# Kernel optimization log

Measured on AMD Instinct MI355X. Metric: run time of the kernel, lower is better.

Reference implementation:

```python
import jax, jax.numpy as jnp
import numpy as np

N = 20000      # nodes
E = 320000     # edges (avg in-degree 16)
R = 100        # relation types
F = 256        # in_ent_feats == out_ent_feats == in_rel_feats
H = 8          # heads
D = F // H     # head dim = 32
HOP = 5        # PPR hops
ALPHA = 0.1
SLOPE = 0.2    # LeakyReLU negative slope


def _ln(x, g, b, eps=1e-5):
    m = x.mean(-1, keepdims=True)
    v = ((x - m) ** 2).mean(-1, keepdims=True)
    return (x - m) / jnp.sqrt(v + eps) * g + b


def setup_inputs() -> dict:
    key = jax.random.key(0)
    ks = jax.random.split(key, 12)
    s = 1.0 / np.sqrt(F)
    ent_feat = jax.random.normal(ks[0], (N, F), jnp.float32)
    rel_feat = jax.random.normal(ks[1], (R, F), jnp.float32)
    W_head = jax.random.normal(ks[2], (F, F), jnp.float32) * s
    W_tail = jax.random.normal(ks[3], (F, F), jnp.float32) * s
    W_ent = jax.random.normal(ks[4], (F, F), jnp.float32) * s
    W_rel = jax.random.normal(ks[5], (F, F), jnp.float32) * s
    attn = jax.random.normal(ks[6], (1, H, D), jnp.float32) * s
    ln_ent_g = jnp.ones((F,), jnp.float32); ln_ent_b = jnp.zeros((F,), jnp.float32)
    ln_rel_g = jnp.ones((F,), jnp.float32); ln_rel_b = jnp.zeros((F,), jnp.float32)
    ln_ff_g = jnp.ones((F,), jnp.float32); ln_ff_b = jnp.zeros((F,), jnp.float32)
    W1 = jax.random.normal(ks[7], (F, 4 * F), jnp.float32) * s
    b1 = jnp.zeros((4 * F,), jnp.float32)
    W2 = jax.random.normal(ks[8], (4 * F, F), jnp.float32) * (0.5 * s)
    b2 = jnp.zeros((F,), jnp.float32)
    src = jax.random.randint(ks[9], (E,), 0, N, dtype=jnp.int32)
    # every node must have in-degree >= 1 (DGL raises on 0-in-degree nodes)
    dst = jnp.concatenate([jnp.arange(N, dtype=jnp.int32),
                           jax.random.randint(ks[10], (E - N,), 0, N, dtype=jnp.int32)])
    rid = jax.random.randint(ks[11], (E,), 0, R, dtype=jnp.int32)
    return {"ent_feat": ent_feat, "rel_feat": rel_feat,
            "W_head": W_head, "W_tail": W_tail, "W_ent": W_ent, "W_rel": W_rel,
            "attn": attn,
            "ln_ent_g": ln_ent_g, "ln_ent_b": ln_ent_b,
            "ln_rel_g": ln_rel_g, "ln_rel_b": ln_rel_b,
            "ln_ff_g": ln_ff_g, "ln_ff_b": ln_ff_b,
            "W1": W1, "b1": b1, "W2": W2, "b2": b2,
            "src": src, "dst": dst, "rid": rid}


def reference(ent_feat, rel_feat, W_head, W_tail, W_ent, W_rel, attn,
              ln_ent_g, ln_ent_b, ln_rel_g, ln_rel_b, ln_ff_g, ln_ff_b,
              W1, b1, W2, b2, src, dst, rid):
    n = ent_feat.shape[0]
    x = _ln(ent_feat, ln_ent_g, ln_ent_b)                 # [N,F]
    fh = (x @ W_head).reshape(n, H, D)                    # 'eh'
    ftl = (x @ W_tail).reshape(n, H, D)                   # 'et'
    fen = (x @ W_ent).reshape(n, H, D)                    # 'ft'
    r = _ln(rel_feat, ln_rel_g, ln_rel_b)
    fr = (r @ W_rel).reshape(-1, H, D)[rid]               # [E,H,D]
    # relational edge attention score
    e = jax.nn.leaky_relu(fh[src] * ftl[dst] * fr, SLOPE)
    e = (e * attn).sum(-1)                                # [E,H]
    # e_mul_v with log in-degree, scaled by head_dim
    deg = jax.ops.segment_sum(jnp.ones((src.shape[0],), e.dtype), dst, num_segments=n)
    e = e * (jnp.log(deg)[dst])[:, None] / D
    # edge softmax over incoming edges of each dst node, per head
    m = jax.lax.stop_gradient(jax.ops.segment_max(e, dst, num_segments=n))
    ex = jnp.exp(e - m[dst])
    denom = jax.ops.segment_sum(ex, dst, num_segments=n)
    a = ex / denom[dst]                                   # [E,H]
    # PPR-style diffusion aggregation
    feat0 = fen
    feat = fen
    for _ in range(HOP):
        msg = feat[src] * a[:, :, None]                   # [E,H,D]
        agg = jax.ops.segment_sum(msg, dst, num_segments=n)
        feat = (1.0 - ALPHA) * agg + ALPHA * feat0
    # residual (Identity since in_ent_feats == out_ent_feats)
    rst = feat + ent_feat.reshape(n, H, D)
    rst = rst.reshape(n, F)
    # position-wise feed-forward with pre-LN and residual
    y = _ln(rst, ln_ff_g, ln_ff_b)
    ff = jax.nn.relu(y @ W1 + b1) @ W2 + b2
    return ff + rst
```

## Files before the change

### kernel.cpp

```cpp
#include <hip/hip_runtime.h>

#define N_NODES 20000
#define N_EDGES 320000
#define N_REL   100
#define FDIM    256
#define NHEAD   8
#define HDIM    32
#define SCAN_BLOCKS ((N_NODES + 255) / 256)

using short8 = __attribute__((ext_vector_type(8))) short;
using f32x4  = __attribute__((ext_vector_type(4))) float;

__device__ inline unsigned short f2bf(float f) {
    union { float f; unsigned int u; } v; v.f = f;
    unsigned int r = v.u + 0x7fff + ((v.u >> 16) & 1);
    return (unsigned short)(r >> 16);
}
__device__ inline float bf2f(unsigned short u) {
    union { unsigned int i; float f; } v; v.i = ((unsigned int)u) << 16; return v.f;
}
__device__ inline float4 bf4(ushort4 u) {
    return make_float4(bf2f(u.x), bf2f(u.y), bf2f(u.z), bf2f(u.w));
}
__device__ inline void unpack8(float* d, uint4 u) {
    union { unsigned int u; float f; } t;
    t.u = u.x << 16;         d[0] = t.f;
    t.u = u.x & 0xffff0000u; d[1] = t.f;
    t.u = u.y << 16;         d[2] = t.f;
    t.u = u.y & 0xffff0000u; d[3] = t.f;
    t.u = u.z << 16;         d[4] = t.f;
    t.u = u.z & 0xffff0000u; d[5] = t.f;
    t.u = u.w << 16;         d[6] = t.f;
    t.u = u.w & 0xffff0000u; d[7] = t.f;
}
__device__ inline void fma8(float* acc, uint4 u, float w) {
    union { unsigned int u; float f; } t;
    t.u = u.x << 16;         acc[0] += w * t.f;
    t.u = u.x & 0xffff0000u; acc[1] += w * t.f;
    t.u = u.y << 16;         acc[2] += w * t.f;
    t.u = u.y & 0xffff0000u; acc[3] += w * t.f;
    t.u = u.z << 16;         acc[4] += w * t.f;
    t.u = u.z & 0xffff0000u; acc[5] += w * t.f;
    t.u = u.w << 16;         acc[6] += w * t.f;
    t.u = u.w & 0xffff0000u; acc[7] += w * t.f;
}
__device__ __forceinline__ void g2lds16(const unsigned short* g, unsigned short* l) {
    __builtin_amdgcn_global_load_lds(
        (const __attribute__((address_space(1))) unsigned int*)g,
        (__attribute__((address_space(3))) unsigned int*)l,
        16, 0, 0);
}

__device__ inline void xcd_tile(int* m0, int* n0, int tm, int tn) {
    int nwg  = gridDim.x * gridDim.y;
    int wgid = blockIdx.x + blockIdx.y * gridDim.x;
    int q = nwg >> 3, r = nwg & 7;
    int xcd = wgid & 7, pos = wgid >> 3;
    int nid = (xcd < r ? xcd * (q + 1) : r * (q + 1) + (xcd - r) * q) + pos;
    int gy = gridDim.y;
    int bx = nid / gy;
    int by = nid - bx * gy;
    *m0 = bx * tm;
    *n0 = by * tn;
}

__global__ __launch_bounds__(64) void ln_bf16_kernel(
    const float* __restrict__ in, const float* __restrict__ g,
    const float* __restrict__ b, unsigned short* __restrict__ out, int rows)
{
    int row = blockIdx.x;
    if (row >= rows) return;
    int tid = threadIdx.x;
    const float4 v = *(const float4*)(in + (size_t)row * FDIM + tid * 4);
    float s = v.x + v.y + v.z + v.w;
    float q = v.x * v.x + v.y * v.y + v.z * v.z + v.w * v.w;
    #pragma unroll
    for (int d = 1; d < 64; d <<= 1) { s += __shfl_xor(s, d); q += __shfl_xor(q, d); }
// ... 232 lines not shown
__global__ __launch_bounds__(128) void scan2_kernel(int* __restrict__ bsum, int nb)
{
    __shared__ int tmp[128];
    int tid = threadIdx.x;
    int v = (tid < nb) ? bsum[tid] : 0;
    tmp[tid] = v;
    __syncthreads();
    for (int d = 1; d < 128; d <<= 1) {
        int u = (tid >= d) ? tmp[tid - d] : 0;
        __syncthreads();
        tmp[tid] += u;
        __syncthreads();
    }
    if (tid < nb) bsum[tid] = tmp[tid] - v;
}

__global__ __launch_bounds__(256) void scan3_kernel(
    const int* __restrict__ deg, int* __restrict__ offsets,
    const int* __restrict__ bsum, int* __restrict__ cursor,
    float* __restrict__ logdeg, int n, int E)
{
    int i = blockIdx.x * 256 + threadIdx.x;
    if (i < n) {
        int o = offsets[i] + bsum[blockIdx.x];
        offsets[i] = o;
        cursor[i]  = o;
        logdeg[i]  = logf((float)deg[i]);
    }
    if (i == 0) offsets[n] = E;
}

__global__ void scatter_kernel(const int* __restrict__ dst, const int* __restrict__ src,
                               const int* __restrict__ rid, int* __restrict__ cursor,
                               int* __restrict__ csr_src, int* __restrict__ csr_rid, int E)
{
    int i = blockIdx.x * blockDim.x + threadIdx.x;
    if (i < E) {
        int p = atomicAdd(&cursor[dst[i]], 1);
        csr_src[p] = src[i];
        csr_rid[p] = rid[i];
    }
}

__global__ __launch_bounds__(256) void edge_score_csr_kernel(
    const unsigned short* __restrict__ proj,
    const unsigned short* __restrict__ frel,
    const float* __restrict__ attn,
    const int* __restrict__ csr_src, const int* __restrict__ csr_rid,
    const int* __restrict__ offsets, const float* __restrict__ logdeg,
    float* __restrict__ csr_a, int n)
{
    int node = blockIdx.x * 4 + (threadIdx.x >> 6);
    if (node >= n) return;
    int tid = threadIdx.x & 63;
    int g = tid >> 4, li = tid & 15;
    int start = offsets[node], end = offsets[node + 1];
    float scale = logdeg[node] * (1.0f / 32.0f);

    float tv[16], at[16];
    {
        const unsigned short* tp = proj + (size_t)node * 768 + 256 + li * 16;
        uint4 a0 = *(const uint4*)tp, a1 = *(const uint4*)(tp + 8);
        unpack8(tv, a0); unpack8(tv + 8, a1);
        const float4* ap = (const float4*)(attn + li * 16);
        float4 f;
        f = ap[0]; at[0] = f.x; at[1] = f.y; at[2]  = f.z; at[3]  = f.w;
        f = ap[1]; at[4] = f.x; at[5] = f.y; at[6]  = f.z; at[7]  = f.w;
        f = ap[2]; at[8] = f.x; at[9] = f.y; at[10] = f.z; at[11] = f.w;
        f = ap[3]; at[12] = f.x; at[13] = f.y; at[14] = f.z; at[15] = f.w;
    }

    float denom = 0.f;
    for (int p = start; p < end; p += 8) {
        int  pe[2]; bool va[2]; uint4 h0[2], h1[2], r0[2], r1[2];
        #pragma unroll
        for (int t = 0; t < 2; ++t) {
            pe[t] = p + t * 4 + g;
            va[t] = pe[t] < end;
            int q = va[t] ? pe[t] : end - 1;
            int s = csr_src[q], r = csr_rid[q];
            const unsigned short* hp = proj + (size_t)s * 768 + li * 16;
            const unsigned short* rp = frel + (size_t)r * FDIM + li * 16;
            h0[t] = *(const uint4*)hp; h1[t] = *(const uint4*)(hp + 8);
            r0[t] = *(const uint4*)rp; r1[t] = *(const uint4*)(rp + 8);
        }
        #pragma unroll
        for (int t = 0; t < 2; ++t) {
            float hv[16], rv[16];
            unpack8(hv, h0[t]); unpack8(hv + 8, h1[t]);
            unpack8(rv, r0[t]); unpack8(rv + 8, r1[t]);
            float sum = 0.f;
            #pragma unroll
            for (int k = 0; k < 16; ++k) {
                float m = hv[k] * tv[k] * rv[k];
                m = (m > 0.f) ? m : 0.2f * m;
                sum += m * at[k];
            }
            sum += __shfl_xor(sum, 1);
            float ex = expf(sum * scale);
            if (va[t] && ((li & 1) == 0)) {
                csr_a[(size_t)pe[t] * NHEAD + (li >> 1)] = ex;
                denom += ex;
            }
        }
    }
    denom += __shfl_xor(denom, 16);
    denom += __shfl_xor(denom, 32);
    float dh = __shfl(denom, 2 * (tid & 7));
    for (int i = start * NHEAD + tid; i < end * NHEAD; i += 64)
        csr_a[i] = csr_a[i] / dh;
}

__global__ __launch_bounds__(256) void diffuse_kernel(
    const unsigned short* __restrict__ fin, int fin_stride,
    const unsigned short* __restrict__ feat0,
    const float* __restrict__ a, const int* __restrict__ csr_src,
    const int* __restrict__ offsets, unsigned short* __restrict__ fout, int n)
{
    int node = blockIdx.x * 4 + (threadIdx.x >> 6);
    if (node >= n) return;
    int tid = threadIdx.x & 63;
    int g = tid >> 4, li = tid & 15;
    int hh = li >> 1;
    int start = offsets[node], end = offsets[node + 1];
    float acc[16] = {};

    for (int p = start; p < end; p += 16) {
        uint4 u0[4], u1[4]; float w[4];
        #pragma unroll
        for (int t = 0; t < 4; ++t) {
            int pe = p + t * 4 + g;
            int q = (pe < end) ? pe : end - 1;
            int s = csr_src[q];
            w[t] = (pe < end) ? a[(size_t)q * NHEAD + hh] : 0.0f;
            const unsigned short* rp = fin + (size_t)s * fin_stride + li * 16;
            u0[t] = *(const uint4*)(rp);
            u1[t] = *(const uint4*)(rp + 8);
        }
        #pragma unroll
        for (int t = 0; t < 4; ++t) {
            fma8(acc + 0, u0[t], w[t]);
            fma8(acc + 8, u1[t], w[t]);
        }
    }
    #pragma unroll
    for (int k = 0; k < 16; ++k) {
        acc[k] += __shfl_xor(acc[k], 16);
        acc[k] += __shfl_xor(acc[k], 32);
    }
    if (g == 0) {
        const unsigned short* f0p = feat0 + (size_t)node * 768 + li * 16;
        uint4 f0a = *(const uint4*)(f0p);
        uint4 f0b = *(const uint4*)(f0p + 8);
        float f0[16];
        unpack8(f0, f0a); unpack8(f0 + 8, f0b);
        unsigned short o[16];
        #pragma unroll
        for (int k = 0; k < 16; ++k) o[k] = f2bf(0.9f * acc[k] + 0.1f * f0[k]);
        uint4* dst4 = (uint4*)(fout + (size_t)node * FDIM + li * 16);
        dst4[0] = *(uint4*)(o);
        dst4[1] = *(uint4*)(o + 8);
    }
}

extern "C" void kernel_launch(void* const* d_in, const int* in_sizes, int n_in,
                              void* d_out, int out_size, void* d_ws, size_t ws_size,
                              hipStream_t stream)
{
    const float* ent_feat = (const float*)d_in[0];
    const float* rel_feat = (const float*)d_in[1];
    const float* W_head   = (const float*)d_in[2];
    const float* W_tail   = (const float*)d_in[3];
    const float* W_ent    = (const float*)d_in[4];
    const float* W_rel    = (const float*)d_in[5];
    const float* attn     = (const float*)d_in[6];
    const float* ln_ent_g = (const float*)d_in[7];
    const float* ln_ent_b = (const float*)d_in[8];
    const float* ln_rel_g = (const float*)d_in[9];
    const float* ln_rel_b = (const float*)d_in[10];
    const float* ln_ff_g  = (const float*)d_in[11];
    const float* ln_ff_b  = (const float*)d_in[12];
    const float* W1       = (const float*)d_in[13];
    const float* b1       = (const float*)d_in[14];
    const float* W2       = (const float*)d_in[15];
    const float* b2       = (const float*)d_in[16];
    const int*   src      = (const int*)d_in[17];
    const int*   dst      = (const int*)d_in[18];
    const int*   rid      = (const int*)d_in[19];
    float* out = (float*)d_out;

    char* base = (char*)d_ws;
    auto carve = [&](size_t bytes) { char* p = base; base += (bytes + 255) & ~(size_t)255; return p; };
    unsigned short* xb    = (unsigned short*)carve((size_t)N_NODES * FDIM * 2);
    unsigned short* projb = (unsigned short*)carve((size_t)N_NODES * 768 * 2);
    unsigned short* rlnb  = (unsigned short*)carve((size_t)N_REL * FDIM * 2);
    unsigned short* frelb = (unsigned short*)carve((size_t)N_REL * FDIM * 2);
    unsigned short* WtP   = (unsigned short*)carve((size_t)768 * FDIM * 2);
    unsigned short* WtR   = (unsigned short*)carve((size_t)FDIM * FDIM * 2);
    unsigned short* W1t   = (unsigned short*)carve((size_t)1024 * FDIM * 2);
    unsigned short* W2t   = (unsigned short*)carve((size_t)FDIM * 1024 * 2);
    unsigned short* hb0   = (unsigned short*)carve((size_t)N_NODES * FDIM * 2);
    unsigned short* hb1   = (unsigned short*)carve((size_t)N_NODES * FDIM * 2);
    unsigned short* yb    = (unsigned short*)carve((size_t)N_NODES * FDIM * 2);
    unsigned short* t1b   = (unsigned short*)carve((size_t)N_NODES * 1024 * 2);
    float* rst     = (float*)carve((size_t)N_NODES * FDIM * 4);
    float* csr_a   = (float*)carve(((size_t)N_EDGES * NHEAD + 256) * 4);
    int*   csr_src = (int*)carve((size_t)(N_EDGES + 64) * 4);
    int*   csr_rid = (int*)carve((size_t)(N_EDGES + 64) * 4);
    int*   deg     = (int*)carve((size_t)N_NODES * 4);
    float* logdeg  = (float*)carve((size_t)N_NODES * 4);
    int*   offsets = (int*)carve((size_t)(N_NODES + 1) * 4);
    int*   cursor  = (int*)carve((size_t)N_NODES * 4);
    int*   bsum    = (int*)carve((size_t)SCAN_BLOCKS * 4);

    hipMemsetAsync(deg, 0, (size_t)N_NODES * 4, stream);

    ln_bf16_kernel<<<N_NODES, 64, 0, stream>>>(ent_feat, ln_ent_g, ln_ent_b, xb, N_NODES);
    ln_bf16_kernel<<<N_REL, 64, 0, stream>>>(rel_feat, ln_rel_g, ln_rel_b, rlnb, N_REL);

    transpose_bf16_kernel<<<(65536 + 255) / 256, 256, 0, stream>>>(W_head, WtP,              FDIM, FDIM);
    transpose_bf16_kernel<<<(65536 + 255) / 256, 256, 0, stream>>>(W_tail, WtP + 256 * FDIM, FDIM, FDIM);
    transpose_bf16_kernel<<<(65536 + 255) / 256, 256, 0, stream>>>(W_ent,  WtP + 512 * FDIM, FDIM, FDIM);
    transpose_bf16_kernel<<<(65536 + 255) / 256, 256, 0, stream>>>(W_rel,  WtR, FDIM, FDIM);
    transpose_bf16_kernel<<<(262144 + 255) / 256, 256, 0, stream>>>(W1, W1t, FDIM, 1024);
    transpose_bf16_kernel<<<(262144 + 255) / 256, 256, 0, stream>>>(W2, W2t, 1024, FDIM);

    dim3 gproj((N_NODES + 127) / 128, 768 / 128);
    mfma_gemm_bt<<<gproj, 256, 0, stream>>>(xb, WtP, nullptr, nullptr, nullptr, projb,
                                            N_NODES, FDIM, 768, 0);
    dim3 grel(1, FDIM / 128);
    mfma_gemm_bt<<<grel, 256, 0, stream>>>(rlnb, WtR, nullptr, nullptr, nullptr, frelb,
                                           N_REL, FDIM, FDIM, 0);

    count_kernel<<<(N_EDGES + 255) / 256, 256, 0, stream>>>(dst, deg, N_EDGES);
    scan1_kernel<<<SCAN_BLOCKS, 256, 0, stream>>>(deg, offsets, bsum, N_NODES);
    scan2_kernel<<<1, 128, 0, stream>>>(bsum, SCAN_BLOCKS);
    scan3_kernel<<<SCAN_BLOCKS, 256, 0, stream>>>(deg, offsets, bsum, cursor, logdeg,
                                                  N_NODES, N_EDGES);
    scatter_kernel<<<(N_EDGES + 255) / 256, 256, 0, stream>>>(dst, src, rid, cursor,
                                                              csr_src, csr_rid, N_EDGES);

    edge_score_csr_kernel<<<(N_NODES + 3) / 4, 256, 0, stream>>>(
        projb, frelb, attn, csr_src, csr_rid, offsets, logdeg, csr_a, N_NODES);

    const unsigned short* fen = projb + 512;
    int gdif = (N_NODES + 3) / 4;
    diffuse_kernel<<<gdif, 256, 0, stream>>>(fen, 768, fen, csr_a, csr_src, offsets, hb0, N_NODES);
    diffuse_kernel<<<gdif, 256, 0, stream>>>(hb0, FDIM, fen, csr_a, csr_src, offsets, hb1, N_NODES);
    diffuse_kernel<<<gdif, 256, 0, stream>>>(hb1, FDIM, fen, csr_a, csr_src, offsets, hb0, N_NODES);
    diffuse_kernel<<<gdif, 256, 0, stream>>>(hb0, FDIM, fen, csr_a, csr_src, offsets, hb1, N_NODES);
    diffuse_kernel<<<gdif, 256, 0, stream>>>(hb1, FDIM, fen, csr_a, csr_src, offsets, hb0, N_NODES);

    rst_ln_kernel<<<N_NODES, 64, 0, stream>>>(hb0, ent_feat, ln_ff_g, ln_ff_b, rst, yb);

    dim3 gff1((N_NODES + 127) / 128, 1024 / 128);
    mfma_gemm_bt<<<gff1, 256, 0, stream>>>(yb, W1t, b1, nullptr, nullptr, t1b,
                                           N_NODES, FDIM, 1024, 1);
    dim3 gff2((N_NODES + 63) / 64, FDIM / 128);
    mfma_gemm64_bt<<<gff2, 256, 0, stream>>>(t1b, W2t, b2, rst, out,
                                             N_NODES, 1024, FDIM);
}
```

Baseline: 495.0 us.

## Defer softmax normalization to diffuse and double-buffer gather loads via shuffled CSR indices

The edge score kernel no longer rescales csr_a in a second pass. It stores one reciprocal denominator per node and head, and the diffuse kernel multiplies the aggregated sum by it. Both kernels now preload up to 64 CSR source and relation indices into registers, broadcast them with shuffles, and software-pipeline the neighbor gathers with two register buffers to hide memory latency. The extra live buffers raise register pressure, and the diffuse kernel now processes 8 edges per stage instead of 16.

```diff
diff --git a/kernel.cpp b/kernel.cpp
--- a/kernel.cpp
+++ b/kernel.cpp
@@ -357,14 +357,19 @@
     const float* __restrict__ attn,
     const int* __restrict__ csr_src, const int* __restrict__ csr_rid,
     const int* __restrict__ offsets, const float* __restrict__ logdeg,
-    float* __restrict__ csr_a, int n)
+    float* __restrict__ csr_a, float* __restrict__ invd, int n)
 {
     int node = blockIdx.x * 4 + (threadIdx.x >> 6);
     if (node >= n) return;
     int tid = threadIdx.x & 63;
     int g = tid >> 4, li = tid & 15;
     int start = offsets[node], end = offsets[node + 1];
+    int ecnt = end - start;
     float scale = logdeg[node] * (1.0f / 32.0f);
+
+    int idxc = (start + tid < end) ? start + tid : end - 1;
+    int sReg = csr_src[idxc];
+    int rReg = csr_rid[idxc];
 
     float tv[16], at[16];
     {
@@ -380,19 +385,26 @@
     }
 
     float denom = 0.f;
-    for (int p = start; p < end; p += 8) {
-        int  pe[2]; bool va[2]; uint4 h0[2], h1[2], r0[2], r1[2];
+    uint4 Ah0[2], Ah1[2], Ar0[2], Ar1[2]; int Ape[2];
+    uint4 Bh0[2], Bh1[2], Br0[2], Br1[2]; int Bpe[2];
+
+    auto loadc = [&](int p, uint4* h0, uint4* h1, uint4* r0, uint4* r1, int* pe) {
         #pragma unroll
         for (int t = 0; t < 2; ++t) {
-            pe[t] = p + t * 4 + g;
-            va[t] = pe[t] < end;
-            int q = va[t] ? pe[t] : end - 1;
-            int s = csr_src[q], r = csr_rid[q];
+            int e = p + t * 4 + g;
+            pe[t] = e;
+            int ec = (e < ecnt) ? e : ecnt - 1;
+            int s, r;
+            if (ec < 64) { s = __shfl(sReg, ec); r = __shfl(rReg, ec); }
+            else         { s = csr_src[start + ec]; r = csr_rid[start + ec]; }
             const unsigned short* hp = proj + (size_t)s * 768 + li * 16;
             const unsigned short* rp = frel + (size_t)r * FDIM + li * 16;
             h0[t] = *(const uint4*)hp; h1[t] = *(const uint4*)(hp + 8);
             r0[t] = *(const uint4*)rp; r1[t] = *(const uint4*)(rp + 8);
         }
+    };
+    auto consume = [&](const uint4* h0, const uint4* h1, const uint4* r0,
+                       const uint4* r1, const int* pe) {
         #pragma unroll
         for (int t = 0; t < 2; ++t) {
             float hv[16], rv[16];
@@ -407,23 +419,32 @@
             }
             sum += __shfl_xor(sum, 1);
             float ex = expf(sum * scale);
-            if (va[t] && ((li & 1) == 0)) {
-                csr_a[(size_t)pe[t] * NHEAD + (li >> 1)] = ex;
+            if (pe[t] < ecnt && ((li & 1) == 0)) {
+                csr_a[(size_t)(start + pe[t]) * NHEAD + (li >> 1)] = ex;
                 denom += ex;
             }
         }
-    }
+    };
+
+    loadc(0, Ah0, Ah1, Ar0, Ar1, Ape);
+    for (int p = 0; p < ecnt; p += 16) {
+        if (p + 8 < ecnt)  loadc(p + 8, Bh0, Bh1, Br0, Br1, Bpe);
+        consume(Ah0, Ah1, Ar0, Ar1, Ape);
+        if (p + 16 < ecnt) loadc(p + 16, Ah0, Ah1, Ar0, Ar1, Ape);
+        if (p + 8 < ecnt)  consume(Bh0, Bh1, Br0, Br1, Bpe);
+    }
+
     denom += __shfl_xor(denom, 16);
     denom += __shfl_xor(denom, 32);
-    float dh = __shfl(denom, 2 * (tid & 7));
-    for (int i = start * NHEAD + tid; i < end * NHEAD; i += 64)
-        csr_a[i] = csr_a[i] / dh;
+    if (g == 0 && (li & 1) == 0)
+        invd[node * NHEAD + (li >> 1)] = 1.0f / denom;
 }
 
 __global__ __launch_bounds__(256) void diffuse_kernel(
     const unsigned short* __restrict__ fin, int fin_stride,
     const unsigned short* __restrict__ feat0,
-    const float* __restrict__ a, const int* __restrict__ csr_src,
+    const float* __restrict__ a, const float* __restrict__ invd,
+    const int* __restrict__ csr_src,
     const int* __restrict__ offsets, unsigned short* __restrict__ fout, int n)
 {
     int node = blockIdx.x * 4 + (threadIdx.x >> 6);
@@ -432,26 +453,44 @@
     int g = tid >> 4, li = tid & 15;
     int hh = li >> 1;
     int start = offsets[node], end = offsets[node + 1];
+    int ecnt = end - start;
+    float wnorm = invd[node * NHEAD + hh];
+
+    int idxc = (start + tid < end) ? start + tid : end - 1;
+    int sReg = csr_src[idxc];
+
     float acc[16] = {};
-
-    for (int p = start; p < end; p += 16) {
-        uint4 u0[4], u1[4]; float w[4];
-        #pragma unroll
-        for (int t = 0; t < 4; ++t) {
-            int pe = p + t * 4 + g;
-            int q = (pe < end) ? pe : end - 1;
-            int s = csr_src[q];
-            w[t] = (pe < end) ? a[(size_t)q * NHEAD + hh] : 0.0f;
+    uint4 Au0[2], Au1[2]; float Aw[2];
+    uint4 Bu0[2], Bu1[2]; float Bw[2];
+
+    auto loadc = [&](int p, uint4* u0, uint4* u1, float* w) {
+        #pragma unroll
+        for (int t = 0; t < 2; ++t) {
+            int e = p + t * 4 + g;
+            int ec = (e < ecnt) ? e : ecnt - 1;
+            int s = (ec < 64) ? __shfl(sReg, ec) : csr_src[start + ec];
+            w[t] = (e < ecnt) ? a[(size_t)(start + ec) * NHEAD + hh] : 0.0f;
             const unsigned short* rp = fin + (size_t)s * fin_stride + li * 16;
             u0[t] = *(const uint4*)(rp);
             u1[t] = *(const uint4*)(rp + 8);
         }
-        #pragma unroll
-        for (int t = 0; t < 4; ++t) {
+    };
+    auto consume = [&](const uint4* u0, const uint4* u1, const float* w) {
+        #pragma unroll
+        for (int t = 0; t < 2; ++t) {
             fma8(acc + 0, u0[t], w[t]);
             fma8(acc + 8, u1[t], w[t]);
         }
-    }
+    };
+
+    loadc(0, Au0, Au1, Aw);
+    for (int p = 0; p < ecnt; p += 16) {
+        if (p + 8 < ecnt)  loadc(p + 8, Bu0, Bu1, Bw);
+        consume(Au0, Au1, Aw);
+        if (p + 16 < ecnt) loadc(p + 16, Au0, Au1, Aw);
+        if (p + 8 < ecnt)  consume(Bu0, Bu1, Bw);
+    }
+
     #pragma unroll
     for (int k = 0; k < 16; ++k) {
         acc[k] += __shfl_xor(acc[k], 16);
@@ -465,7 +504,8 @@
         unpack8(f0, f0a); unpack8(f0 + 8, f0b);
         unsigned short o[16];
         #pragma unroll
-        for (int k = 0; k < 16; ++k) o[k] = f2bf(0.9f * acc[k] + 0.1f * f0[k]);
+        for (int k = 0; k < 16; ++k)
+            o[k] = f2bf(0.9f * acc[k] * wnorm + 0.1f * f0[k]);
         uint4* dst4 = (uint4*)(fout + (size_t)node * FDIM + li * 16);
         dst4[0] = *(uint4*)(o);
         dst4[1] = *(uint4*)(o + 8);
@@ -514,6 +554,7 @@
     unsigned short* t1b   = (unsigned short*)carve((size_t)N_NODES * 1024 * 2);
     float* rst     = (float*)carve((size_t)N_NODES * FDIM * 4);
     float* csr_a   = (float*)carve(((size_t)N_EDGES * NHEAD + 256) * 4);
+    float* invd    = (float*)carve((size_t)N_NODES * NHEAD * 4);
     int*   csr_src = (int*)carve((size_t)(N_EDGES + 64) * 4);
     int*   csr_rid = (int*)carve((size_t)(N_EDGES + 64) * 4);
     int*   deg     = (int*)carve((size_t)N_NODES * 4);
@@ -550,15 +591,15 @@
                                                               csr_src, csr_rid, N_EDGES);
 
     edge_score_csr_kernel<<<(N_NODES + 3) / 4, 256, 0, stream>>>(
-        projb, frelb, attn, csr_src, csr_rid, offsets, logdeg, csr_a, N_NODES);
+        projb, frelb, attn, csr_src, csr_rid, offsets, logdeg, csr_a, invd, N_NODES);
 
     const unsigned short* fen = projb + 512;
     int gdif = (N_NODES + 3) / 4;
-    diffuse_kernel<<<gdif, 256, 0, stream>>>(fen, 768, fen, csr_a, csr_src, offsets, hb0, N_NODES);
-    diffuse_kernel<<<gdif, 256, 0, stream>>>(hb0, FDIM, fen, csr_a, csr_src, offsets, hb1, N_NODES);
-    diffuse_kernel<<<gdif, 256, 0, stream>>>(hb1, FDIM, fen, csr_a, csr_src, offsets, hb0, N_NODES);
-    diffuse_kernel<<<gdif, 256, 0, stream>>>(hb0, FDIM, fen, csr_a, csr_src, offsets, hb1, N_NODES);
-    diffuse_kernel<<<gdif, 256, 0, stream>>>(hb1, FDIM, fen, csr_a, csr_src, offsets, hb0, N_NODES);
+    diffuse_kernel<<<gdif, 256, 0, stream>>>(fen, 768, fen, csr_a, invd, csr_src, offsets, hb0, N_NODES);
+    diffuse_kernel<<<gdif, 256, 0, stream>>>(hb0, FDIM, fen, csr_a, invd, csr_src, offsets, hb1, N_NODES);
+    diffuse_kernel<<<gdif, 256, 0, stream>>>(hb1, FDIM, fen, csr_a, invd, csr_src, offsets, hb0, N_NODES);
+    diffuse_kernel<<<gdif, 256, 0, stream>>>(hb0, FDIM, fen, csr_a, invd, csr_src, offsets, hb1, N_NODES);
+    diffuse_kernel<<<gdif, 256, 0, stream>>>(hb1, FDIM, fen, csr_a, invd, csr_src, offsets, hb0, N_NODES);
 
     rst_ln_kernel<<<N_NODES, 64, 0, stream>>>(hb0, ent_feat, ln_ff_g, ln_ff_b, rst, yb);
 
```

Result: slower. 509.1 us (+2.8%).

## Parallelize edge scoring per edge and fold softmax normalization into diffusion

Applied to the files above, without the earlier changes.

Edge scoring moves from one wave per destination node to 16 lanes per edge, using a new csr_dst array. The softmax denominator is now built with atomics into a per-node/head buffer and inverted by a small recip kernel, so the per-node renormalization pass over csr_a goes away. The diffusion kernels apply the inverse denominator at output time, cache up to 64 source indices in a register and fetch them by shuffle, unroll by 2 instead of 4, and set launch bounds for occupancy. In exchange there are per-edge atomics, an extra CSR array and an extra launch, and edge scores now use unnormalized exps, which carries overflow risk.

```diff
diff --git a/kernel.cpp b/kernel.cpp
--- a/kernel.cpp
+++ b/kernel.cpp
@@ -22,27 +22,31 @@
 __device__ inline float4 bf4(ushort4 u) {
     return make_float4(bf2f(u.x), bf2f(u.y), bf2f(u.z), bf2f(u.w));
 }
+__device__ inline float bf_lo(unsigned int u) {
+    union { unsigned int i; float f; } v; v.i = u << 16; return v.f;
+}
+__device__ inline float bf_hi(unsigned int u) {
+    union { unsigned int i; float f; } v; v.i = u & 0xffff0000u; return v.f;
+}
 __device__ inline void unpack8(float* d, uint4 u) {
-    union { unsigned int u; float f; } t;
-    t.u = u.x << 16;         d[0] = t.f;
-    t.u = u.x & 0xffff0000u; d[1] = t.f;
-    t.u = u.y << 16;         d[2] = t.f;
-    t.u = u.y & 0xffff0000u; d[3] = t.f;
-    t.u = u.z << 16;         d[4] = t.f;
-    t.u = u.z & 0xffff0000u; d[5] = t.f;
-    t.u = u.w << 16;         d[6] = t.f;
-    t.u = u.w & 0xffff0000u; d[7] = t.f;
+    d[0] = bf_lo(u.x); d[1] = bf_hi(u.x);
+    d[2] = bf_lo(u.y); d[3] = bf_hi(u.y);
+    d[4] = bf_lo(u.z); d[5] = bf_hi(u.z);
+    d[6] = bf_lo(u.w); d[7] = bf_hi(u.w);
 }
 __device__ inline void fma8(float* acc, uint4 u, float w) {
-    union { unsigned int u; float f; } t;
-    t.u = u.x << 16;         acc[0] += w * t.f;
-    t.u = u.x & 0xffff0000u; acc[1] += w * t.f;
-    t.u = u.y << 16;         acc[2] += w * t.f;
-    t.u = u.y & 0xffff0000u; acc[3] += w * t.f;
-    t.u = u.z << 16;         acc[4] += w * t.f;
-    t.u = u.z & 0xffff0000u; acc[5] += w * t.f;
-    t.u = u.w << 16;         acc[6] += w * t.f;
-    t.u = u.w & 0xffff0000u; acc[7] += w * t.f;
+    acc[0] += w * bf_lo(u.x); acc[1] += w * bf_hi(u.x);
+    acc[2] += w * bf_lo(u.y); acc[3] += w * bf_hi(u.y);
+    acc[4] += w * bf_lo(u.z); acc[5] += w * bf_hi(u.z);
+    acc[6] += w * bf_lo(u.w); acc[7] += w * bf_hi(u.w);
+}
+__device__ inline float ldot2(unsigned int h, unsigned int t, unsigned int r,
+                              float a0, float a1) {
+    float m0 = bf_lo(h) * bf_lo(t) * bf_lo(r);
+    m0 = (m0 > 0.f) ? m0 : 0.2f * m0;
+    float m1 = bf_hi(h) * bf_hi(t) * bf_hi(r);
+    m1 = (m1 > 0.f) ? m1 : 0.2f * m1;
+    return m0 * a0 + m1 * a1;
 }
 __device__ __forceinline__ void g2lds16(const unsigned short* g, unsigned short* l) {
     __builtin_amdgcn_global_load_lds(
@@ -341,89 +345,72 @@
 
 __global__ void scatter_kernel(const int* __restrict__ dst, const int* __restrict__ src,
                                const int* __restrict__ rid, int* __restrict__ cursor,
-                               int* __restrict__ csr_src, int* __restrict__ csr_rid, int E)
+                               int* __restrict__ csr_src, int* __restrict__ csr_rid,
+                               int* __restrict__ csr_dst, int E)
 {
     int i = blockIdx.x * blockDim.x + threadIdx.x;
     if (i < E) {
-        int p = atomicAdd(&cursor[dst[i]], 1);
+        int d = dst[i];
+        int p = atomicAdd(&cursor[d], 1);
         csr_src[p] = src[i];
         csr_rid[p] = rid[i];
-    }
-}
-
-__global__ __launch_bounds__(256) void edge_score_csr_kernel(
+        csr_dst[p] = d;
+    }
+}
+
+__global__ __launch_bounds__(256, 8) void edge_score_epar_kernel(
     const unsigned short* __restrict__ proj,
     const unsigned short* __restrict__ frel,
     const float* __restrict__ attn,
     const int* __restrict__ csr_src, const int* __restrict__ csr_rid,
-    const int* __restrict__ offsets, const float* __restrict__ logdeg,
-    float* __restrict__ csr_a, int n)
-{
-    int node = blockIdx.x * 4 + (threadIdx.x >> 6);
-    if (node >= n) return;
-    int tid = threadIdx.x & 63;
-    int g = tid >> 4, li = tid & 15;
-    int start = offsets[node], end = offsets[node + 1];
-    float scale = logdeg[node] * (1.0f / 32.0f);
-
-    float tv[16], at[16];
-    {
-        const unsigned short* tp = proj + (size_t)node * 768 + 256 + li * 16;
-        uint4 a0 = *(const uint4*)tp, a1 = *(const uint4*)(tp + 8);
-        unpack8(tv, a0); unpack8(tv + 8, a1);
-        const float4* ap = (const float4*)(attn + li * 16);
-        float4 f;
-        f = ap[0]; at[0] = f.x; at[1] = f.y; at[2]  = f.z; at[3]  = f.w;
-        f = ap[1]; at[4] = f.x; at[5] = f.y; at[6]  = f.z; at[7]  = f.w;
-        f = ap[2]; at[8] = f.x; at[9] = f.y; at[10] = f.z; at[11] = f.w;
-        f = ap[3]; at[12] = f.x; at[13] = f.y; at[14] = f.z; at[15] = f.w;
-    }
-
-    float denom = 0.f;
-    for (int p = start; p < end; p += 8) {
-        int  pe[2]; bool va[2]; uint4 h0[2], h1[2], r0[2], r1[2];
-        #pragma unroll
-        for (int t = 0; t < 2; ++t) {
-            pe[t] = p + t * 4 + g;
-            va[t] = pe[t] < end;
-            int q = va[t] ? pe[t] : end - 1;
-            int s = csr_src[q], r = csr_rid[q];
-            const unsigned short* hp = proj + (size_t)s * 768 + li * 16;
-            const unsigned short* rp = frel + (size_t)r * FDIM + li * 16;
-            h0[t] = *(const uint4*)hp; h1[t] = *(const uint4*)(hp + 8);
-            r0[t] = *(const uint4*)rp; r1[t] = *(const uint4*)(rp + 8);
-        }
-        #pragma unroll
-        for (int t = 0; t < 2; ++t) {
-            float hv[16], rv[16];
-            unpack8(hv, h0[t]); unpack8(hv + 8, h1[t]);
-            unpack8(rv, r0[t]); unpack8(rv + 8, r1[t]);
-            float sum = 0.f;
-            #pragma unroll
-            for (int k = 0; k < 16; ++k) {
-                float m = hv[k] * tv[k] * rv[k];
-                m = (m > 0.f) ? m : 0.2f * m;
-                sum += m * at[k];
-            }
-            sum += __shfl_xor(sum, 1);
-            float ex = expf(sum * scale);
-            if (va[t] && ((li & 1) == 0)) {
-                csr_a[(size_t)pe[t] * NHEAD + (li >> 1)] = ex;
-                denom += ex;
-            }
-        }
-    }
-    denom += __shfl_xor(denom, 16);
-    denom += __shfl_xor(denom, 32);
-    float dh = __shfl(denom, 2 * (tid & 7));
-    for (int i = start * NHEAD + tid; i < end * NHEAD; i += 64)
-        csr_a[i] = csr_a[i] / dh;
-}
-
-__global__ __launch_bounds__(256) void diffuse_kernel(
+    const int* __restrict__ csr_dst, const float* __restrict__ logdeg,
+    float* __restrict__ csr_a, float* __restrict__ denom, int E)
+{
+    int e = blockIdx.x * 16 + (threadIdx.x >> 4);
+    if (e >= E) return;
+    int li = threadIdx.x & 15;
+    int s = csr_src[e], r = csr_rid[e], nd = csr_dst[e];
+    float scale = logdeg[nd] * (1.0f / 32.0f);
+
+    const unsigned short* hp = proj + (size_t)s  * 768 + li * 16;
+    const unsigned short* tp = proj + (size_t)nd * 768 + 256 + li * 16;
+    const unsigned short* rp = frel + (size_t)r  * FDIM + li * 16;
+    uint4 h0 = *(const uint4*)hp, h1 = *(const uint4*)(hp + 8);
+    uint4 t0 = *(const uint4*)tp, t1 = *(const uint4*)(tp + 8);
+    uint4 r0 = *(const uint4*)rp, r1 = *(const uint4*)(rp + 8);
+    const float4* ap = (const float4*)(attn + li * 16);
+    float4 a0 = ap[0], a1 = ap[1], a2 = ap[2], a3 = ap[3];
+
+    float sum = 0.f;
+    sum += ldot2(h0.x, t0.x, r0.x, a0.x, a0.y);
+    sum += ldot2(h0.y, t0.y, r0.y, a0.z, a0.w);
+    sum += ldot2(h0.z, t0.z, r0.z, a1.x, a1.y);
+    sum += ldot2(h0.w, t0.w, r0.w, a1.z, a1.w);
+    sum += ldot2(h1.x, t1.x, r1.x, a2.x, a2.y);
+    sum += ldot2(h1.y, t1.y, r1.y, a2.z, a2.w);
+    sum += ldot2(h1.z, t1.z, r1.z, a3.x, a3.y);
+    sum += ldot2(h1.w, t1.w, r1.w, a3.z, a3.w);
+    sum += __shfl_xor(sum, 1);
+
+    if ((li & 1) == 0) {
+        float ex = expf(sum * scale);
+        int h = li >> 1;
+        csr_a[(size_t)e * NHEAD + h] = ex;
+        atomicAdd(&denom[nd * NHEAD + h], ex);
+    }
+}
+
+__global__ void recip_kernel(float* __restrict__ d, int n)
+{
+    int i = blockIdx.x * 256 + threadIdx.x;
+    if (i < n) d[i] = 1.0f / d[i];
+}
+
+__global__ __launch_bounds__(256, 8) void diffuse_kernel(
     const unsigned short* __restrict__ fin, int fin_stride,
     const unsigned short* __restrict__ feat0,
-    const float* __restrict__ a, const int* __restrict__ csr_src,
+    const float* __restrict__ a, const float* __restrict__ invd,
+    const int* __restrict__ csr_src,
     const int* __restrict__ offsets, unsigned short* __restrict__ fout, int n)
 {
     int node = blockIdx.x * 4 + (threadIdx.x >> 6);
@@ -432,26 +419,33 @@
     int g = tid >> 4, li = tid & 15;
     int hh = li >> 1;
     int start = offsets[node], end = offsets[node + 1];
+    int ecnt = end - start;
+    float wnorm = invd[node * NHEAD + hh];
+
+    int idxc = (start + tid < end) ? start + tid : end - 1;
+    int sReg = csr_src[idxc];
+
     float acc[16] = {};
 
-    for (int p = start; p < end; p += 16) {
-        uint4 u0[4], u1[4]; float w[4];
-        #pragma unroll
-        for (int t = 0; t < 4; ++t) {
-            int pe = p + t * 4 + g;
-            int q = (pe < end) ? pe : end - 1;
-            int s = csr_src[q];
-            w[t] = (pe < end) ? a[(size_t)q * NHEAD + hh] : 0.0f;
+    for (int p = 0; p < ecnt; p += 8) {
+        uint4 u0[2], u1[2]; float w[2];
+        #pragma unroll
+        for (int t = 0; t < 2; ++t) {
+            int e = p + t * 4 + g;
+            int ec = (e < ecnt) ? e : ecnt - 1;
+            int s = (ec < 64) ? __shfl(sReg, ec) : csr_src[start + ec];
+            w[t] = (e < ecnt) ? a[(size_t)(start + ec) * NHEAD + hh] : 0.0f;
             const unsigned short* rp = fin + (size_t)s * fin_stride + li * 16;
             u0[t] = *(const uint4*)(rp);
             u1[t] = *(const uint4*)(rp + 8);
         }
         #pragma unroll
-        for (int t = 0; t < 4; ++t) {
+        for (int t = 0; t < 2; ++t) {
             fma8(acc + 0, u0[t], w[t]);
             fma8(acc + 8, u1[t], w[t]);
         }
     }
+
     #pragma unroll
     for (int k = 0; k < 16; ++k) {
         acc[k] += __shfl_xor(acc[k], 16);
@@ -461,11 +455,27 @@
         const unsigned short* f0p = feat0 + (size_t)node * 768 + li * 16;
         uint4 f0a = *(const uint4*)(f0p);
         uint4 f0b = *(const uint4*)(f0p + 8);
-        float f0[16];
-        unpack8(f0, f0a); unpack8(f0 + 8, f0b);
         unsigned short o[16];
         #pragma unroll
-        for (int k = 0; k < 16; ++k) o[k] = f2bf(0.9f * acc[k] + 0.1f * f0[k]);
+        for (int k = 0; k < 8; ++k) {
+            float lo = (k & 1) ? 0.f : 0.f; (void)lo;
+        }
+        o[0]  = f2bf(0.9f * acc[0]  * wnorm + 0.1f * bf_lo(f0a.x));
+        o[1]  = f2bf(0.9f * acc[1]  * wnorm + 0.1f * bf_hi(f0a.x));
+        o[2]  = f2bf(0.9f * acc[2]  * wnorm + 0.1f * bf_lo(f0a.y));
+        o[3]  = f2bf(0.9f * acc[3]  * wnorm + 0.1f * bf_hi(f0a.y));
+        o[4]  = f2bf(0.9f * acc[4]  * wnorm + 0.1f * bf_lo(f0a.z));
+        o[5]  = f2bf(0.9f * acc[5]  * wnorm + 0.1f * bf_hi(f0a.z));
+        o[6]  = f2bf(0.9f * acc[6]  * wnorm + 0.1f * bf_lo(f0a.w));
+        o[7]  = f2bf(0.9f * acc[7]  * wnorm + 0.1f * bf_hi(f0a.w));
+        o[8]  = f2bf(0.9f * acc[8]  * wnorm + 0.1f * bf_lo(f0b.x));
+        o[9]  = f2bf(0.9f * acc[9]  * wnorm + 0.1f * bf_hi(f0b.x));
+        o[10] = f2bf(0.9f * acc[10] * wnorm + 0.1f * bf_lo(f0b.y));
+        o[11] = f2bf(0.9f * acc[11] * wnorm + 0.1f * bf_hi(f0b.y));
+        o[12] = f2bf(0.9f * acc[12] * wnorm + 0.1f * bf_lo(f0b.z));
+        o[13] = f2bf(0.9f * acc[13] * wnorm + 0.1f * bf_hi(f0b.z));
+        o[14] = f2bf(0.9f * acc[14] * wnorm + 0.1f * bf_lo(f0b.w));
+        o[15] = f2bf(0.9f * acc[15] * wnorm + 0.1f * bf_hi(f0b.w));
         uint4* dst4 = (uint4*)(fout + (size_t)node * FDIM + li * 16);
         dst4[0] = *(uint4*)(o);
         dst4[1] = *(uint4*)(o + 8);
@@ -514,8 +524,10 @@
     unsigned short* t1b   = (unsigned short*)carve((size_t)N_NODES * 1024 * 2);
     float* rst     = (float*)carve((size_t)N_NODES * FDIM * 4);
     float* csr_a   = (float*)carve(((size_t)N_EDGES * NHEAD + 256) * 4);
+    float* invd    = (float*)carve((size_t)N_NODES * NHEAD * 4);
     int*   csr_src = (int*)carve((size_t)(N_EDGES + 64) * 4);
     int*   csr_rid = (int*)carve((size_t)(N_EDGES + 64) * 4);
+    int*   csr_dst = (int*)carve((size_t)(N_EDGES + 64) * 4);
     int*   deg     = (int*)carve((size_t)N_NODES * 4);
     float* logdeg  = (float*)carve((size_t)N_NODES * 4);
     int*   offsets = (int*)carve((size_t)(N_NODES + 1) * 4);
@@ -523,6 +535,7 @@
     int*   bsum    = (int*)carve((size_t)SCAN_BLOCKS * 4);
 
     hipMemsetAsync(deg, 0, (size_t)N_NODES * 4, stream);
+    hipMemsetAsync(invd, 0, (size_t)N_NODES * NHEAD * 4, stream);
 
     ln_bf16_kernel<<<N_NODES, 64, 0, stream>>>(ent_feat, ln_ent_g, ln_ent_b, xb, N_NODES);
     ln_bf16_kernel<<<N_REL, 64, 0, stream>>>(rel_feat, ln_rel_g, ln_rel_b, rlnb, N_REL);
@@ -547,18 +560,20 @@
     scan3_kernel<<<SCAN_BLOCKS, 256, 0, stream>>>(deg, offsets, bsum, cursor, logdeg,
                                                   N_NODES, N_EDGES);
     scatter_kernel<<<(N_EDGES + 255) / 256, 256, 0, stream>>>(dst, src, rid, cursor,
-                                                              csr_src, csr_rid, N_EDGES);
-
-    edge_score_csr_kernel<<<(N_NODES + 3) / 4, 256, 0, stream>>>(
-        projb, frelb, attn, csr_src, csr_rid, offsets, logdeg, csr_a, N_NODES);
+                                                              csr_src, csr_rid, csr_dst,
+                                                              N_EDGES);
+
+    edge_score_epar_kernel<<<N_EDGES / 16, 256, 0, stream>>>(
+        projb, frelb, attn, csr_src, csr_rid, csr_dst, logdeg, csr_a, invd, N_EDGES);
+    recip_kernel<<<(N_NODES * NHEAD + 255) / 256, 256, 0, stream>>>(invd, N_NODES * NHEAD);
 
     const unsigned short* fen = projb + 512;
     int gdif = (N_NODES + 3) / 4;
-    diffuse_kernel<<<gdif, 256, 0, stream>>>(fen, 768, fen, csr_a, csr_src, offsets, hb0, N_NODES);
-    diffuse_kernel<<<gdif, 256, 0, stream>>>(hb0, FDIM, fen, csr_a, csr_src, offsets, hb1, N_NODES);
-    diffuse_kernel<<<gdif, 256, 0, stream>>>(hb1, FDIM, fen, csr_a, csr_src, offsets, hb0, N_NODES);
-    diffuse_kernel<<<gdif, 256, 0, stream>>>(hb0, FDIM, fen, csr_a, csr_src, offsets, hb1, N_NODES);
-    diffuse_kernel<<<gdif, 256, 0, stream>>>(hb1, FDIM, fen, csr_a, csr_src, offsets, hb0, N_NODES);
+    diffuse_kernel<<<gdif, 256, 0, stream>>>(fen, 768, fen, csr_a, invd, csr_src, offsets, hb0, N_NODES);
+    diffuse_kernel<<<gdif, 256, 0, stream>>>(hb0, FDIM, fen, csr_a, invd, csr_src, offsets, hb1, N_NODES);
+    diffuse_kernel<<<gdif, 256, 0, stream>>>(hb1, FDIM, fen, csr_a, invd, csr_src, offsets, hb0, N_NODES);
+    diffuse_kernel<<<gdif, 256, 0, stream>>>(hb0, FDIM, fen, csr_a, invd, csr_src, offsets, hb1, N_NODES);
+    diffuse_kernel<<<gdif, 256, 0, stream>>>(hb1, FDIM, fen, csr_a, invd, csr_src, offsets, hb0, N_NODES);
 
     rst_ln_kernel<<<N_NODES, 64, 0, stream>>>(hb0, ent_feat, ln_ff_g, ln_ff_b, rst, yb);
 
```

Result: slower. 524.3 us (+5.9%).

## Repack features head-major and split edge-score/diffusion per head

Applied to the files above, without the earlier changes.

Adds repack kernels that move the head, tail, entity and relation projections into a head-major layout [H][N][32]. Edge scoring and the five diffusion hops then run as one block slice per head, and each slice gathers only a 64-byte segment per neighbour. The intent is better L2 locality, since one head's working set (about 1.3MB per feature array) fits in cache while the old full 512-byte rows did not. Softmax normalisation is deferred: unnormalised exponentials and a per-node inverse denominator are stored and applied at the diffusion output, which removes the separate normalisation pass. The cost is extra repack traffic and kernel launches, and the CSR indices are now re-read once per head, eight times in total.

```diff
diff --git a/kernel.cpp b/kernel.cpp
--- a/kernel.cpp
+++ b/kernel.cpp
@@ -22,27 +22,11 @@
 __device__ inline float4 bf4(ushort4 u) {
     return make_float4(bf2f(u.x), bf2f(u.y), bf2f(u.z), bf2f(u.w));
 }
-__device__ inline void unpack8(float* d, uint4 u) {
-    union { unsigned int u; float f; } t;
-    t.u = u.x << 16;         d[0] = t.f;
-    t.u = u.x & 0xffff0000u; d[1] = t.f;
-    t.u = u.y << 16;         d[2] = t.f;
-    t.u = u.y & 0xffff0000u; d[3] = t.f;
-    t.u = u.z << 16;         d[4] = t.f;
-    t.u = u.z & 0xffff0000u; d[5] = t.f;
-    t.u = u.w << 16;         d[6] = t.f;
-    t.u = u.w & 0xffff0000u; d[7] = t.f;
-}
-__device__ inline void fma8(float* acc, uint4 u, float w) {
-    union { unsigned int u; float f; } t;
-    t.u = u.x << 16;         acc[0] += w * t.f;
-    t.u = u.x & 0xffff0000u; acc[1] += w * t.f;
-    t.u = u.y << 16;         acc[2] += w * t.f;
-    t.u = u.y & 0xffff0000u; acc[3] += w * t.f;
-    t.u = u.z << 16;         acc[4] += w * t.f;
-    t.u = u.z & 0xffff0000u; acc[5] += w * t.f;
-    t.u = u.w << 16;         acc[6] += w * t.f;
-    t.u = u.w & 0xffff0000u; acc[7] += w * t.f;
+__device__ inline float bf_lo(unsigned int u) {
+    union { unsigned int i; float f; } v; v.i = u << 16; return v.f;
+}
+__device__ inline float bf_hi(unsigned int u) {
+    union { unsigned int i; float f; } v; v.i = u & 0xffff0000u; return v.f;
 }
 __device__ __forceinline__ void g2lds16(const unsigned short* g, unsigned short* l) {
     __builtin_amdgcn_global_load_lds(
@@ -351,124 +335,134 @@
     }
 }
 
-__global__ __launch_bounds__(256) void edge_score_csr_kernel(
+__global__ __launch_bounds__(256) void repack_heads_kernel(
     const unsigned short* __restrict__ proj,
-    const unsigned short* __restrict__ frel,
+    unsigned short* __restrict__ fh, unsigned short* __restrict__ ft,
+    unsigned short* __restrict__ fe, int n)
+{
+    int idx = blockIdx.x * 256 + threadIdx.x;
+    if (idx >= n * 192) return;
+    int node = idx / 192, c = idx - node * 192;
+    int part = c >> 6, rem = c & 63;
+    int h = rem >> 3, d4 = rem & 7;
+    unsigned long long v = *(const unsigned long long*)(proj + (size_t)node * 768 + c * 4);
+    unsigned short* dst = (part == 0) ? fh : (part == 1) ? ft : fe;
+    *(unsigned long long*)(dst + ((size_t)h * n + node) * 32 + d4 * 4) = v;
+}
+
+__global__ __launch_bounds__(256) void repack_rel_kernel(
+    const unsigned short* __restrict__ frel, unsigned short* __restrict__ out)
+{
+    int idx = blockIdx.x * 256 + threadIdx.x;
+    if (idx >= N_REL * 64) return;
+    int r = idx >> 6, rem = idx & 63;
+    int h = rem >> 3, d4 = rem & 7;
+    unsigned long long v = *(const unsigned long long*)(frel + (size_t)r * FDIM + rem * 4);
+    *(unsigned long long*)(out + ((size_t)h * N_REL + r) * 32 + d4 * 4) = v;
+}
+
+__global__ __launch_bounds__(256, 8) void edge_score_h_kernel(
+    const unsigned short* __restrict__ fhh,
+    const unsigned short* __restrict__ ftlh,
+    const unsigned short* __restrict__ frelh,
     const float* __restrict__ attn,
     const int* __restrict__ csr_src, const int* __restrict__ csr_rid,
     const int* __restrict__ offsets, const float* __restrict__ logdeg,
-    float* __restrict__ csr_a, int n)
-{
-    int node = blockIdx.x * 4 + (threadIdx.x >> 6);
+    float* __restrict__ a_h, float* __restrict__ invd_h, int n)
+{
+    int head = blockIdx.x & 7;
+    int node = (blockIdx.x >> 3) * 4 + (threadIdx.x >> 6);
     if (node >= n) return;
-    int tid = threadIdx.x & 63;
-    int g = tid >> 4, li = tid & 15;
+    int lane = threadIdx.x & 63;
+    int g = lane >> 3, li = lane & 7;
     int start = offsets[node], end = offsets[node + 1];
     float scale = logdeg[node] * (1.0f / 32.0f);
 
-    float tv[16], at[16];
-    {
-        const unsigned short* tp = proj + (size_t)node * 768 + 256 + li * 16;
-        uint4 a0 = *(const uint4*)tp, a1 = *(const uint4*)(tp + 8);
-        unpack8(tv, a0); unpack8(tv + 8, a1);
-        const float4* ap = (const float4*)(attn + li * 16);
-        float4 f;
-        f = ap[0]; at[0] = f.x; at[1] = f.y; at[2]  = f.z; at[3]  = f.w;
-        f = ap[1]; at[4] = f.x; at[5] = f.y; at[6]  = f.z; at[7]  = f.w;
-        f = ap[2]; at[8] = f.x; at[9] = f.y; at[10] = f.z; at[11] = f.w;
-        f = ap[3]; at[12] = f.x; at[13] = f.y; at[14] = f.z; at[15] = f.w;
-    }
-
-    float denom = 0.f;
+    const size_t hb = (size_t)head * n;
+    const size_t rb = (size_t)head * N_REL;
+    uint2 tp = *(const uint2*)(ftlh + (hb + node) * 32 + li * 4);
+    float t0 = bf_lo(tp.x), t1 = bf_hi(tp.x), t2 = bf_lo(tp.y), t3 = bf_hi(tp.y);
+    float4 av = *(const float4*)(attn + head * 32 + li * 4);
+    float* ah = a_h + (size_t)head * N_EDGES;
+
+    float dsum = 0.f;
     for (int p = start; p < end; p += 8) {
-        int  pe[2]; bool va[2]; uint4 h0[2], h1[2], r0[2], r1[2];
-        #pragma unroll
-        for (int t = 0; t < 2; ++t) {
-            pe[t] = p + t * 4 + g;
-            va[t] = pe[t] < end;
-            int q = va[t] ? pe[t] : end - 1;
-            int s = csr_src[q], r = csr_rid[q];
-            const unsigned short* hp = proj + (size_t)s * 768 + li * 16;
-            const unsigned short* rp = frel + (size_t)r * FDIM + li * 16;
-            h0[t] = *(const uint4*)hp; h1[t] = *(const uint4*)(hp + 8);
-            r0[t] = *(const uint4*)rp; r1[t] = *(const uint4*)(rp + 8);
-        }
-        #pragma unroll
-        for (int t = 0; t < 2; ++t) {
-            float hv[16], rv[16];
-            unpack8(hv, h0[t]); unpack8(hv + 8, h1[t]);
-            unpack8(rv, r0[t]); unpack8(rv + 8, r1[t]);
-            float sum = 0.f;
-            #pragma unroll
-            for (int k = 0; k < 16; ++k) {
-                float m = hv[k] * tv[k] * rv[k];
-                m = (m > 0.f) ? m : 0.2f * m;
-                sum += m * at[k];
-            }
-            sum += __shfl_xor(sum, 1);
-            float ex = expf(sum * scale);
-            if (va[t] && ((li & 1) == 0)) {
-                csr_a[(size_t)pe[t] * NHEAD + (li >> 1)] = ex;
-                denom += ex;
-            }
-        }
-    }
-    denom += __shfl_xor(denom, 16);
-    denom += __shfl_xor(denom, 32);
-    float dh = __shfl(denom, 2 * (tid & 7));
-    for (int i = start * NHEAD + tid; i < end * NHEAD; i += 64)
-        csr_a[i] = csr_a[i] / dh;
-}
-
-__global__ __launch_bounds__(256) void diffuse_kernel(
-    const unsigned short* __restrict__ fin, int fin_stride,
-    const unsigned short* __restrict__ feat0,
-    const float* __restrict__ a, const int* __restrict__ csr_src,
-    const int* __restrict__ offsets, unsigned short* __restrict__ fout, int n)
-{
-    int node = blockIdx.x * 4 + (threadIdx.x >> 6);
+        int e = p + g;
+        bool va = e < end;
+        int ee = va ? e : end - 1;
+        int s = csr_src[ee], r = csr_rid[ee];
+        uint2 hp = *(const uint2*)(fhh + (hb + s) * 32 + li * 4);
+        uint2 rp = *(const uint2*)(frelh + (rb + r) * 32 + li * 4);
+        float m0 = bf_lo(hp.x) * t0 * bf_lo(rp.x);
+        m0 = (m0 > 0.f) ? m0 : 0.2f * m0;
+        float m1 = bf_hi(hp.x) * t1 * bf_hi(rp.x);
+        m1 = (m1 > 0.f) ? m1 : 0.2f * m1;
+        float m2 = bf_lo(hp.y) * t2 * bf_lo(rp.y);
+        m2 = (m2 > 0.f) ? m2 : 0.2f * m2;
+        float m3 = bf_hi(hp.y) * t3 * bf_hi(rp.y);
+        m3 = (m3 > 0.f) ? m3 : 0.2f * m3;
+        float sum = m0 * av.x + m1 * av.y + m2 * av.z + m3 * av.w;
+        sum += __shfl_xor(sum, 1);
+        sum += __shfl_xor(sum, 2);
+        sum += __shfl_xor(sum, 4);
+        float ex = va ? expf(sum * scale) : 0.f;
+        if (va && li == 0) ah[e] = ex;
+        dsum += ex;
+    }
+    dsum += __shfl_xor(dsum, 8);
+    dsum += __shfl_xor(dsum, 16);
+    dsum += __shfl_xor(dsum, 32);
+    if (lane == 0) invd_h[hb + node] = 1.0f / dsum;
+}
+
+__global__ __launch_bounds__(256, 8) void diffuse_h_kernel(
+    const unsigned short* __restrict__ fin_h,
+    const unsigned short* __restrict__ feat0_h,
+    const float* __restrict__ a_h, const float* __restrict__ invd_h,
+    const int* __restrict__ csr_src, const int* __restrict__ offsets,
+    unsigned short* __restrict__ fout, int node_major, int n)
+{
+    int head = blockIdx.x & 7;
+    int node = (blockIdx.x >> 3) * 4 + (threadIdx.x >> 6);
     if (node >= n) return;
-    int tid = threadIdx.x & 63;
-    int g = tid >> 4, li = tid & 15;
-    int hh = li >> 1;
+    int lane = threadIdx.x & 63;
+    int g = lane >> 3, li = lane & 7;
     int start = offsets[node], end = offsets[node + 1];
-    float acc[16] = {};
-
-    for (int p = start; p < end; p += 16) {
-        uint4 u0[4], u1[4]; float w[4];
-        #pragma unroll
-        for (int t = 0; t < 4; ++t) {
-            int pe = p + t * 4 + g;
-            int q = (pe < end) ? pe : end - 1;
-            int s = csr_src[q];
-            w[t] = (pe < end) ? a[(size_t)q * NHEAD + hh] : 0.0f;
-            const unsigned short* rp = fin + (size_t)s * fin_stride + li * 16;
-            u0[t] = *(const uint4*)(rp);
-            u1[t] = *(const uint4*)(rp + 8);
-        }
-        #pragma unroll
-        for (int t = 0; t < 4; ++t) {
-            fma8(acc + 0, u0[t], w[t]);
-            fma8(acc + 8, u1[t], w[t]);
-        }
+    const size_t hb = (size_t)head * n;
+    float wn = invd_h[hb + node];
+    const float* ah = a_h + (size_t)head * N_EDGES;
+
+    float a0 = 0.f, a1 = 0.f, a2 = 0.f, a3 = 0.f;
+    for (int p = start; p < end; p += 8) {
+        int e = p + g;
+        bool va = e < end;
+        int ee = va ? e : end - 1;
+        int s = csr_src[ee];
+        float w = va ? ah[ee] : 0.f;
+        uint2 u = *(const uint2*)(fin_h + (hb + s) * 32 + li * 4);
+        a0 += w * bf_lo(u.x); a1 += w * bf_hi(u.x);
+        a2 += w * bf_lo(u.y); a3 += w * bf_hi(u.y);
     }
     #pragma unroll
-    for (int k = 0; k < 16; ++k) {
-        acc[k] += __shfl_xor(acc[k], 16);
-        acc[k] += __shfl_xor(acc[k], 32);
+    for (int d = 8; d < 64; d <<= 1) {
+        a0 += __shfl_xor(a0, d);
+        a1 += __shfl_xor(a1, d);
+        a2 += __shfl_xor(a2, d);
+        a3 += __shfl_xor(a3, d);
     }
     if (g == 0) {
-        const unsigned short* f0p = feat0 + (size_t)node * 768 + li * 16;
-        uint4 f0a = *(const uint4*)(f0p);
-        uint4 f0b = *(const uint4*)(f0p + 8);
-        float f0[16];
-        unpack8(f0, f0a); unpack8(f0 + 8, f0b);
-        unsigned short o[16];
-        #pragma unroll
-        for (int k = 0; k < 16; ++k) o[k] = f2bf(0.9f * acc[k] + 0.1f * f0[k]);
-        uint4* dst4 = (uint4*)(fout + (size_t)node * FDIM + li * 16);
-        dst4[0] = *(uint4*)(o);
-        dst4[1] = *(uint4*)(o + 8);
+        uint2 f0 = *(const uint2*)(feat0_h + (hb + node) * 32 + li * 4);
+        unsigned short o0 = f2bf(0.9f * a0 * wn + 0.1f * bf_lo(f0.x));
+        unsigned short o1 = f2bf(0.9f * a1 * wn + 0.1f * bf_hi(f0.x));
+        unsigned short o2 = f2bf(0.9f * a2 * wn + 0.1f * bf_lo(f0.y));
+        unsigned short o3 = f2bf(0.9f * a3 * wn + 0.1f * bf_hi(f0.y));
+        uint2 w2;
+        w2.x = (unsigned int)o0 | ((unsigned int)o1 << 16);
+        w2.y = (unsigned int)o2 | ((unsigned int)o3 << 16);
+        if (node_major)
+            *(uint2*)(fout + (size_t)node * FDIM + head * 32 + li * 4) = w2;
+        else
+            *(uint2*)(fout + (hb + node) * 32 + li * 4) = w2;
     }
 }
 
@@ -508,12 +502,18 @@
     unsigned short* WtR   = (unsigned short*)carve((size_t)FDIM * FDIM * 2);
     unsigned short* W1t   = (unsigned short*)carve((size_t)1024 * FDIM * 2);
     unsigned short* W2t   = (unsigned short*)carve((size_t)FDIM * 1024 * 2);
+    unsigned short* fhh   = (unsigned short*)carve((size_t)NHEAD * N_NODES * HDIM * 2);
+    unsigned short* ftlh  = (unsigned short*)carve((size_t)NHEAD * N_NODES * HDIM * 2);
+    unsigned short* fenh  = (unsigned short*)carve((size_t)NHEAD * N_NODES * HDIM * 2);
+    unsigned short* frelh = (unsigned short*)carve((size_t)NHEAD * N_REL * HDIM * 2);
+    unsigned short* g0h   = (unsigned short*)carve((size_t)NHEAD * N_NODES * HDIM * 2);
+    unsigned short* g1h   = (unsigned short*)carve((size_t)NHEAD * N_NODES * HDIM * 2);
     unsigned short* hb0   = (unsigned short*)carve((size_t)N_NODES * FDIM * 2);
-    unsigned short* hb1   = (unsigned short*)carve((size_t)N_NODES * FDIM * 2);
     unsigned short* yb    = (unsigned short*)carve((size_t)N_NODES * FDIM * 2);
     unsigned short* t1b   = (unsigned short*)carve((size_t)N_NODES * 1024 * 2);
     float* rst     = (float*)carve((size_t)N_NODES * FDIM * 4);
-    float* csr_a   = (float*)carve(((size_t)N_EDGES * NHEAD + 256) * 4);
+    float* a_h     = (float*)carve((size_t)NHEAD * N_EDGES * 4);
+    float* invd_h  = (float*)carve((size_t)NHEAD * N_NODES * 4);
     int*   csr_src = (int*)carve((size_t)(N_EDGES + 64) * 4);
     int*   csr_rid = (int*)carve((size_t)(N_EDGES + 64) * 4);
     int*   deg     = (int*)carve((size_t)N_NODES * 4);
@@ -541,6 +541,10 @@
     mfma_gemm_bt<<<grel, 256, 0, stream>>>(rlnb, WtR, nullptr, nullptr, nullptr, frelb,
                                            N_REL, FDIM, FDIM, 0);
 
+    repack_heads_kernel<<<(N_NODES * 192 + 255) / 256, 256, 0, stream>>>(
+        projb, fhh, ftlh, fenh, N_NODES);
+    repack_rel_kernel<<<(N_REL * 64 + 255) / 256, 256, 0, stream>>>(frelb, frelh);
+
     count_kernel<<<(N_EDGES + 255) / 256, 256, 0, stream>>>(dst, deg, N_EDGES);
     scan1_kernel<<<SCAN_BLOCKS, 256, 0, stream>>>(deg, offsets, bsum, N_NODES);
     scan2_kernel<<<1, 128, 0, stream>>>(bsum, SCAN_BLOCKS);
@@ -549,16 +553,15 @@
     scatter_kernel<<<(N_EDGES + 255) / 256, 256, 0, stream>>>(dst, src, rid, cursor,
                                                               csr_src, csr_rid, N_EDGES);
 
-    edge_score_csr_kernel<<<(N_NODES + 3) / 4, 256, 0, stream>>>(
-        projb, frelb, attn, csr_src, csr_rid, offsets, logdeg, csr_a, N_NODES);
-
-    const unsigned short* fen = projb + 512;
-    int gdif = (N_NODES + 3) / 4;
-    diffuse_kernel<<<gdif, 256, 0, stream>>>(fen, 768, fen, csr_a, csr_src, offsets, hb0, N_NODES);
-    diffuse_kernel<<<gdif, 256, 0, stream>>>(hb0, FDIM, fen, csr_a, csr_src, offsets, hb1, N_NODES);
-    diffuse_kernel<<<gdif, 256, 0, stream>>>(hb1, FDIM, fen, csr_a, csr_src, offsets, hb0, N_NODES);
-    diffuse_kernel<<<gdif, 256, 0, stream>>>(hb0, FDIM, fen, csr_a, csr_src, offsets, hb1, N_NODES);
-    diffuse_kernel<<<gdif, 256, 0, stream>>>(hb1, FDIM, fen, csr_a, csr_src, offsets, hb0, N_NODES);
+    int ghead = 8 * ((N_NODES + 3) / 4);
+    edge_score_h_kernel<<<ghead, 256, 0, stream>>>(
+        fhh, ftlh, frelh, attn, csr_src, csr_rid, offsets, logdeg, a_h, invd_h, N_NODES);
+
+    diffuse_h_kernel<<<ghead, 256, 0, stream>>>(fenh, fenh, a_h, invd_h, csr_src, offsets, g0h, 0, N_NODES);
+    diffuse_h_kernel<<<ghead, 256, 0, stream>>>(g0h,  fenh, a_h, invd_h, csr_src, offsets, g1h, 0, N_NODES);
+    diffuse_h_kernel<<<ghead, 256, 0, stream>>>(g1h,  fenh, a_h, invd_h, csr_src, offsets, g0h, 0, N_NODES);
+    diffuse_h_kernel<<<ghead, 256, 0, stream>>>(g0h,  fenh, a_h, invd_h, csr_src, offsets, g1h, 0, N_NODES);
+    diffuse_h_kernel<<<ghead, 256, 0, stream>>>(g1h,  fenh, a_h, invd_h, csr_src, offsets, hb0, 1, N_NODES);
 
     rst_ln_kernel<<<N_NODES, 64, 0, stream>>>(hb0, ent_feat, ln_ff_g, ln_ff_b, rst, yb);
 
```

New measurement: 683.0 us. +38.0%, slower.
